# Optimization experiments

Measured on AMD Instinct MI355X. Metric: run time of the kernel, lower is better.

## Reference

```python
import jax, jax.numpy as jnp
import numpy as np
from jax import lax

WINDOW_SIZE = 11
SIGMA = 1.5
C1 = 0.01 ** 2
C2 = 0.03 ** 2


def _gaussian_window_2d(window_size, sigma):
    # matches torch.linspace(-ws//2+1, ws//2, ws) -> integers -5..5 for ws=11
    lo = -(window_size // 2) + 1 if window_size % 2 == 0 else -(window_size // 2)
    xs = np.linspace(-(window_size // 2) + 1 - (0 if window_size % 2 else 0), window_size // 2, window_size)
    # For ws=11: -(-11//2)+... torch computes linspace(-ws//2+1, ws//2, ws) with Python floor div:
    start = -(window_size // 2) if False else (-window_size) // 2 + 1
    xs = np.linspace(start, window_size // 2, window_size)
    g = np.exp(-(xs ** 2) / (2.0 * sigma ** 2))
    g = g / g.sum()
    w2d = np.outer(g, g).astype(np.float32)  # [ws, ws]
    return w2d


def _depthwise_conv(x, w2d, channel):
    # x: [B, C, H, W]; depthwise 'SAME' conv with shared gaussian kernel
    kernel = jnp.broadcast_to(jnp.asarray(w2d)[None, None], (channel, 1, w2d.shape[0], w2d.shape[1]))
    return lax.conv_general_dilated(
        x, kernel, window_strides=(1, 1), padding='SAME',
        feature_group_count=channel,
        dimension_numbers=('NCHW', 'OIHW', 'NCHW'))


def setup_inputs() -> dict:
    key = jax.random.key(0)
    k1, k2 = jax.random.split(key)
    img1 = jax.random.uniform(k1, (16, 3, 512, 512), dtype=jnp.float32)
    img2 = jax.random.uniform(k2, (16, 3, 512, 512), dtype=jnp.float32)
    return {"img1": img1, "img2": img2}


def reference(img1, img2):
    channel = img1.shape[1]
    w2d = _gaussian_window_2d(WINDOW_SIZE, SIGMA)

    mu1 = _depthwise_conv(img1, w2d, channel)
    mu2 = _depthwise_conv(img2, w2d, channel)
    sigma1_sq = _depthwise_conv(img1 * img1, w2d, channel) - mu1 * mu1
    sigma2_sq = _depthwise_conv(img2 * img2, w2d, channel) - mu2 * mu2
    sigma12 = _depthwise_conv(img1 * img2, w2d, channel) - mu1 * mu2

    ssim_map = ((2 * mu1 * mu2 + C1) * (2 * sigma12 + C2)) / (
        (mu1 * mu1 + mu2 * mu2 + C1) * (sigma1_sq + sigma2_sq + C2))
    return ssim_map.mean()
```

## Files before the change

kernel.cpp:

```cpp
#include <hip/hip_runtime.h>
#include <cstdint>

#define IMG_H 512
#define IMG_W 512
#define ROW_BYTES (IMG_W * 4)
#define NPLANES 48
#define PLANE_SZ (IMG_H * IMG_W)
#define N_ELEM (NPLANES * PLANE_SZ)

#define TILE_W 48
#define TILE_H 32
#define GX 11
#define GY 16
#define NBLOCKS (GX * GY * NPLANES)
#define VPITCH 59

#define SSIM_C1 1e-4f
#define SSIM_C2 9e-4f

typedef int rsrc_t __attribute__((ext_vector_type(4)));
__device__ float
llvm_amdgcn_raw_buffer_load_fp32(rsrc_t srsrc, int voffset, int soffset,
                                 int glc_slc) __asm("llvm.amdgcn.raw.buffer.load.f32");

__device__ inline rsrc_t make_rsrc(const void* p, int bytes) {
    rsrc_t r;
    r.x = (int)(uint32_t)(uintptr_t)p;
    r.y = (int)((uintptr_t)p >> 32);
    r.z = bytes;
    r.w = 0x00020000;
    return r;
}

__global__ __launch_bounds__(256, 4) void ssim_tile_kernel(
    const float* __restrict__ img1, const float* __restrict__ img2,
    double* __restrict__ partials)
{
    __shared__ float4 vs[TILE_H][VPITCH];
    __shared__ double wred[4];

    const float gw[11] = {0.00102838f, 0.00759876f, 0.03600077f, 0.10936069f,
                          0.21300553f, 0.26601172f, 0.21300553f, 0.10936069f,
                          0.03600077f, 0.00759876f, 0.00102838f};

    const int tid  = threadIdx.x;
    const int lane = tid & 63;
    const int wv   = tid >> 6;
    const int ox = blockIdx.x * TILE_W;
    const int oy = blockIdx.y * TILE_H;

    const float* p1 = img1 + (size_t)blockIdx.z * PLANE_SZ;
    const float* p2 = img2 + (size_t)blockIdx.z * PLANE_SZ;
    const rsrc_t rr1 = make_rsrc(p1, PLANE_SZ * 4);
    const rsrc_t rr2 = make_rsrc(p2, PLANE_SZ * 4);

    {
        const int r0 = wv * 8;
        const int srow0 = __builtin_amdgcn_readfirstlane(oy + r0 - 5);
        const int gcol = ox + lane - 5;
        const int coff = ((unsigned)gcol < (unsigned)IMG_W) ? (gcol * 4) : 0x48000000;

        float xs[18], ys[18];
        #pragma unroll
        for (int i = 0; i < 18; ++i) {
            const int soff = (srow0 + i) * ROW_BYTES;
            xs[i] = llvm_amdgcn_raw_buffer_load_fp32(rr1, coff, soff, 0);
            ys[i] = llvm_amdgcn_raw_buffer_load_fp32(rr2, coff, soff, 0);
        }

        float4 acc[8];
        #pragma unroll
        for (int o = 0; o < 8; ++o) acc[o] = make_float4(0.f, 0.f, 0.f, 0.f);
        #pragma unroll
        for (int i = 0; i < 18; ++i) {
            const float s = xs[i] + ys[i], d = xs[i] - ys[i];
            const float s2 = s * s, d2 = d * d;
            #pragma unroll
            for (int o = 0; o < 8; ++o) {
                const int k = i - o;
                if (k >= 0 && k <= 10) {
                    const float w = gw[k];
                    acc[o].x = fmaf(w, s,  acc[o].x);
                    acc[o].y = fmaf(w, d,  acc[o].y);
                    acc[o].z = fmaf(w, s2, acc[o].z);
                    acc[o].w = fmaf(w, d2, acc[o].w);
                }
            }
        }
        if (lane < 58) {
            #pragma unroll
            for (int o = 0; o < 8; ++o) vs[r0 + o][lane] = acc[o];
        }
    }
    __syncthreads();

    float lsum = 0.f;
    {
        const int r  = tid >> 3;
        const int c0 = (tid & 7) * 6;
        float4 m[6];
        #pragma unroll
        for (int j = 0; j < 6; ++j) m[j] = make_float4(0.f, 0.f, 0.f, 0.f);
        #pragma unroll
        for (int t = 0; t < 16; ++t) {
            const float4 v = vs[r][c0 + t];
            #pragma unroll
            for (int j = 0; j < 6; ++j) {
                const int k = t - j;
                if (k >= 0 && k <= 10) {
                    const float w = gw[k];
                    m[j].x = fmaf(w, v.x, m[j].x);
                    m[j].y = fmaf(w, v.y, m[j].y);
                    m[j].z = fmaf(w, v.z, m[j].z);
                    m[j].w = fmaf(w, v.w, m[j].w);
                }
            }
        }
        #pragma unroll
        for (int j = 0; j < 6; ++j) {
            if (ox + c0 + j < IMG_W) {
                const float mus = m[j].x, mud = m[j].y;
                const float es2 = m[j].z, ed2 = m[j].w;
                const float a = mus * mus, b = mud * mud;
                const float num1 = (a - b) * 0.5f + SSIM_C1;
                const float den1 = (a + b) * 0.5f + SSIM_C1;
                const float num2 = (es2 - ed2 - (a - b)) * 0.5f + SSIM_C2;
                const float den2 = (es2 + ed2 - (a + b)) * 0.5f + SSIM_C2;
                lsum += (num1 * num2) * __builtin_amdgcn_rcpf(den1 * den2);
            }
        }
    }

    #pragma unroll
    for (int off = 32; off > 0; off >>= 1)
        lsum += __shfl_down(lsum, off, 64);
    if (lane == 0) wred[wv] = (double)lsum;
    __syncthreads();
    if (tid == 0) {
        const int bid = blockIdx.x + GX * (blockIdx.y + GY * blockIdx.z);
        partials[bid] = wred[0] + wred[1] + wred[2] + wred[3];
    }
}

__global__ __launch_bounds__(1024) void ssim_finalize_kernel(
    const double* __restrict__ partials, float* __restrict__ out)
{
    __shared__ double wred[16];
    const int tid  = threadIdx.x;
    const int lane = tid & 63;
    const int wv   = tid >> 6;
    double s = 0.0;
    #pragma unroll
    for (int i = 0; i < 9; ++i) {
        const int idx = tid + i * 1024;
        if (idx < NBLOCKS) s += partials[idx];
    }
    #pragma unroll
    for (int off = 32; off > 0; off >>= 1)
        s += __shfl_down(s, off, 64);
    if (lane == 0) wred[wv] = s;
    __syncthreads();
    if (wv == 0) {
        double v = (lane < 16) ? wred[lane] : 0.0;
        v += __shfl_down(v, 8, 64);
        v += __shfl_down(v, 4, 64);
        v += __shfl_down(v, 2, 64);
        v += __shfl_down(v, 1, 64);
        if (lane == 0) out[0] = (float)(v / (double)N_ELEM);
    }
}

extern "C" void kernel_launch(void* const* d_in, const int* in_sizes, int n_in,
                              void* d_out, int out_size, void* d_ws, size_t ws_size,
                              hipStream_t stream)
{
    const float* img1 = (const float*)d_in[0];
    const float* img2 = (const float*)d_in[1];
    double* partials  = (double*)d_ws;
    float* out        = (float*)d_out;

    dim3 grid(GX, GY, NPLANES);
    ssim_tile_kernel<<<grid, dim3(256), 0, stream>>>(img1, img2, partials);
    ssim_finalize_kernel<<<1, dim3(1024), 0, stream>>>(partials, out);
}
```

Before: 136.3 us.

## Use packed FMA, make tile passes wave-local, and drop block barriers

```diff
diff --git a/kernel.cpp b/kernel.cpp
--- a/kernel.cpp
+++ b/kernel.cpp
@@ -13,10 +13,13 @@
 #define GX 11
 #define GY 16
 #define NBLOCKS (GX * GY * NPLANES)
+#define NPART (NBLOCKS * 4)
 #define VPITCH 59
 
 #define SSIM_C1 1e-4f
 #define SSIM_C2 9e-4f
+
+typedef float v2f __attribute__((ext_vector_type(2)));
 
 typedef int rsrc_t __attribute__((ext_vector_type(4)));
 __device__ float
@@ -32,12 +35,11 @@
     return r;
 }
 
-__global__ __launch_bounds__(256, 4) void ssim_tile_kernel(
+__global__ __launch_bounds__(256, 5) void ssim_tile_kernel(
     const float* __restrict__ img1, const float* __restrict__ img2,
-    double* __restrict__ partials)
+    float* __restrict__ partials)
 {
     __shared__ float4 vs[TILE_H][VPITCH];
-    __shared__ double wred[4];
 
     const float gw[11] = {0.00102838f, 0.00759876f, 0.03600077f, 0.10936069f,
                           0.21300553f, 0.26601172f, 0.21300553f, 0.10936069f,
@@ -46,6 +48,7 @@
     const int tid  = threadIdx.x;
     const int lane = tid & 63;
     const int wv   = tid >> 6;
+    const int r0   = wv * 8;
     const int ox = blockIdx.x * TILE_W;
     const int oy = blockIdx.y * TILE_H;
 
@@ -55,7 +58,6 @@
     const rsrc_t rr2 = make_rsrc(p2, PLANE_SZ * 4);
 
     {
-        const int r0 = wv * 8;
         const int srow0 = __builtin_amdgcn_readfirstlane(oy + r0 - 5);
         const int gcol = ox + lane - 5;
         const int coff = ((unsigned)gcol < (unsigned)IMG_W) ? (gcol * 4) : 0x48000000;
@@ -68,59 +70,58 @@
             ys[i] = llvm_amdgcn_raw_buffer_load_fp32(rr2, coff, soff, 0);
         }
 
-        float4 acc[8];
+        v2f accP[8], accQ[8];
         #pragma unroll
-        for (int o = 0; o < 8; ++o) acc[o] = make_float4(0.f, 0.f, 0.f, 0.f);
+        for (int o = 0; o < 8; ++o) { accP[o] = (v2f)(0.f); accQ[o] = (v2f)(0.f); }
         #pragma unroll
         for (int i = 0; i < 18; ++i) {
-            const float s = xs[i] + ys[i], d = xs[i] - ys[i];
-            const float s2 = s * s, d2 = d * d;
+            v2f P; P.x = xs[i] + ys[i]; P.y = xs[i] - ys[i];
+            const v2f Q = P * P;
             #pragma unroll
             for (int o = 0; o < 8; ++o) {
                 const int k = i - o;
                 if (k >= 0 && k <= 10) {
-                    const float w = gw[k];
-                    acc[o].x = fmaf(w, s,  acc[o].x);
-                    acc[o].y = fmaf(w, d,  acc[o].y);
-                    acc[o].z = fmaf(w, s2, acc[o].z);
-                    acc[o].w = fmaf(w, d2, acc[o].w);
+                    const v2f w2 = (v2f)(gw[k]);
+                    accP[o] = __builtin_elementwise_fma(P, w2, accP[o]);
+                    accQ[o] = __builtin_elementwise_fma(Q, w2, accQ[o]);
                 }
             }
         }
         if (lane < 58) {
             #pragma unroll
-            for (int o = 0; o < 8; ++o) vs[r0 + o][lane] = acc[o];
+            for (int o = 0; o < 8; ++o)
+                vs[r0 + o][lane] = make_float4(accP[o].x, accP[o].y,
+                                               accQ[o].x, accQ[o].y);
         }
     }
-    __syncthreads();
 
     float lsum = 0.f;
     {
-        const int r  = tid >> 3;
-        const int c0 = (tid & 7) * 6;
-        float4 m[6];
+        const int r  = r0 + (lane >> 3);
+        const int c0 = (lane & 7) * 6;
+        v2f mP[6], mQ[6];
         #pragma unroll
-        for (int j = 0; j < 6; ++j) m[j] = make_float4(0.f, 0.f, 0.f, 0.f);
+        for (int j = 0; j < 6; ++j) { mP[j] = (v2f)(0.f); mQ[j] = (v2f)(0.f); }
         #pragma unroll
         for (int t = 0; t < 16; ++t) {
             const float4 v = vs[r][c0 + t];
+            v2f vP; vP.x = v.x; vP.y = v.y;
+            v2f vQ; vQ.x = v.z; vQ.y = v.w;
             #pragma unroll
             for (int j = 0; j < 6; ++j) {
                 const int k = t - j;
                 if (k >= 0 && k <= 10) {
-                    const float w = gw[k];
-                    m[j].x = fmaf(w, v.x, m[j].x);
-                    m[j].y = fmaf(w, v.y, m[j].y);
-                    m[j].z = fmaf(w, v.z, m[j].z);
-                    m[j].w = fmaf(w, v.w, m[j].w);
+                    const v2f w2 = (v2f)(gw[k]);
+                    mP[j] = __builtin_elementwise_fma(vP, w2, mP[j]);
+                    mQ[j] = __builtin_elementwise_fma(vQ, w2, mQ[j]);
                 }
             }
         }
         #pragma unroll
         for (int j = 0; j < 6; ++j) {
             if (ox + c0 + j < IMG_W) {
-                const float mus = m[j].x, mud = m[j].y;
-                const float es2 = m[j].z, ed2 = m[j].w;
+                const float mus = mP[j].x, mud = mP[j].y;
+                const float es2 = mQ[j].x, ed2 = mQ[j].y;
                 const float a = mus * mus, b = mud * mud;
                 const float num1 = (a - b) * 0.5f + SSIM_C1;
                 const float den1 = (a + b) * 0.5f + SSIM_C1;
@@ -134,16 +135,14 @@
     #pragma unroll
     for (int off = 32; off > 0; off >>= 1)
         lsum += __shfl_down(lsum, off, 64);
-    if (lane == 0) wred[wv] = (double)lsum;
-    __syncthreads();
-    if (tid == 0) {
+    if (lane == 0) {
         const int bid = blockIdx.x + GX * (blockIdx.y + GY * blockIdx.z);
-        partials[bid] = wred[0] + wred[1] + wred[2] + wred[3];
+        partials[(bid << 2) | wv] = lsum;
     }
 }
 
 __global__ __launch_bounds__(1024) void ssim_finalize_kernel(
-    const double* __restrict__ partials, float* __restrict__ out)
+    const float* __restrict__ partials, float* __restrict__ out)
 {
     __shared__ double wred[16];
     const int tid  = threadIdx.x;
@@ -151,10 +150,8 @@
     const int wv   = tid >> 6;
     double s = 0.0;
     #pragma unroll
-    for (int i = 0; i < 9; ++i) {
-        const int idx = tid + i * 1024;
-        if (idx < NBLOCKS) s += partials[idx];
-    }
+    for (int i = 0; i < 33; ++i)
+        s += (double)partials[tid + i * 1024];
     #pragma unroll
     for (int off = 32; off > 0; off >>= 1)
         s += __shfl_down(s, off, 64);
@@ -176,7 +173,7 @@
 {
     const float* img1 = (const float*)d_in[0];
     const float* img2 = (const float*)d_in[1];
-    double* partials  = (double*)d_ws;
+    float* partials   = (float*)d_ws;
     float* out        = (float*)d_out;
 
     dim3 grid(GX, GY, NPLANES);
```

New measurement: 136.5 us. About the same (+0.1%).
